# Kernel tuning notes

Measured on AMD Instinct MI355X. Metric: run time of the kernel, lower is better.

## Reference

```python
import jax, jax.numpy as jnp
import numpy as np

B, S, D, UNITS = 32, 2048, 1024, 1024


def setup_inputs() -> dict:
    key = jax.random.key(0)
    ks = jax.random.split(key, 8)
    scale_d = 1.0 / np.sqrt(D)
    scale_u = 1.0 / np.sqrt(UNITS)
    return {
        "query": jax.random.normal(ks[0], (B, D), jnp.float32),
        "values": jax.random.normal(ks[1], (B, S, D), jnp.float32),
        "W1": jax.random.normal(ks[2], (D, UNITS), jnp.float32) * scale_d,
        "b1": jnp.zeros((UNITS,), jnp.float32),
        "W2": jax.random.normal(ks[3], (D, UNITS), jnp.float32) * scale_d,
        "b2": jnp.zeros((UNITS,), jnp.float32),
        "V": jax.random.normal(ks[4], (UNITS, 1), jnp.float32) * scale_u,
        "bV": jnp.zeros((1,), jnp.float32),
    }


def reference(query, values, W1, b1, W2, b2, V, bV):
    # proj of encoder outputs: [B, S, UNITS]
    proj_v = jnp.einsum("bsd,du->bsu", values, W1) + b1
    # proj of query (hidden), broadcast over sequence: [B, 1, UNITS]
    proj_q = (query @ W2 + b2)[:, None, :]
    # scalar score per position: [B, S, 1]
    score = jnp.tanh(proj_v + proj_q) @ V + bV
    # softmax over the sequence axis (axis=1)
    attention_weights = jax.nn.softmax(score, axis=1)  # [B, S, 1]
    # weighted sum of values: [B, D]
    context_vector = jnp.sum(attention_weights * values, axis=1)
    return context_vector, attention_weights
```

## Files before the change

kernel.cpp:

```cpp
#include <hip/hip_runtime.h>
#include <stdint.h>

typedef float f32x4 __attribute__((ext_vector_type(4)));
typedef short bf16x8 __attribute__((ext_vector_type(8)));
typedef _Float16 f16x8 __attribute__((ext_vector_type(8)));

#define AS1 __attribute__((address_space(1)))
#define AS3 __attribute__((address_space(3)))

#define NB 32
#define NS 2048
#define ND 1024
#define NU 1024
#define NM (NB * NS)

__device__ __forceinline__ void glds16(const void* g, void* l) {
  __builtin_amdgcn_global_load_lds((const AS1 uint32_t*)g, (AS3 uint32_t*)l, 16, 0, 0);
}

__device__ __forceinline__ unsigned short bf16_rne(float f) {
  uint32_t u = __float_as_uint(f);
  u += 0x7fffu + ((u >> 16) & 1u);
  return (unsigned short)(u >> 16);
}

__device__ __forceinline__ uint32_t h2pack(float lo, float hi) {
  union { _Float16 h[2]; uint32_t u; } p;
  p.h[0] = (_Float16)lo;
  p.h[1] = (_Float16)hi;
  return p.u;
}

__device__ __forceinline__ uint32_t pack_bf16_trunc(float lo, float hi) {
  return __builtin_amdgcn_perm(__float_as_uint(hi), __float_as_uint(lo), 0x07060302u);
}

__device__ __forceinline__ float fast_tanh(float x) {
  float e = __expf(2.0f * x);
  return 1.0f - 2.0f / (e + 1.0f);
}

__global__ __launch_bounds__(256) void k_cvt(const float* __restrict__ values,
                                             _Float16* __restrict__ values_h) {
  const size_t gid = (size_t)blockIdx.x * 256 + threadIdx.x;
#pragma unroll 2
  for (int it = 0; it < 8; ++it) {
    const size_t e0 = gid * 8 + (size_t)it * 8388608;
    f32x4 v0 = *(const f32x4*)(values + e0);
    f32x4 v1 = *(const f32x4*)(values + e0 + 4);
    uint4 o;
    o.x = h2pack(v0.x, v0.y);
    o.y = h2pack(v0.z, v0.w);
    o.z = h2pack(v1.x, v1.y);
    o.w = h2pack(v1.z, v1.w);
    *(uint4*)(values_h + e0) = o;
  }
}

__global__ __launch_bounds__(256) void k_w1t_h(const float* __restrict__ W1,
                                               _Float16* __restrict__ W1T) {
  __shared__ float t[64][65];
  const int n0 = blockIdx.x * 64, k0 = blockIdx.y * 64;
  const int tid = threadIdx.x;
  {
    const int r = tid >> 4, c4 = (tid & 15) << 2;
#pragma unroll
    for (int i = 0; i < 4; ++i) {
      f32x4 v = *(const f32x4*)(W1 + (size_t)(k0 + r + i * 16) * NU + n0 + c4);
      t[r + i * 16][c4 + 0] = v.x;
      t[r + i * 16][c4 + 1] = v.y;
      t[r + i * 16][c4 + 2] = v.z;
      t[r + i * 16][c4 + 3] = v.w;
    }
  }
  __syncthreads();
  const int rr = tid >> 2, cc = tid & 3;
  uint32_t o[8];
#pragma unroll
  for (int p = 0; p < 8; ++p)
    o[p] = h2pack(t[cc * 16 + 2 * p + 0][rr], t[cc * 16 + 2 * p + 1][rr]);
  _Float16* dst = W1T + (size_t)(n0 + rr) * ND + k0 + cc * 16;
  *(uint4*)(dst + 0) = make_uint4(o[0], o[1], o[2], o[3]);
  *(uint4*)(dst + 8) = make_uint4(o[4], o[5], o[6], o[7]);
}

__global__ __launch_bounds__(256) void k_w1t(const float* __restrict__ W1,
                                             unsigned short* __restrict__ W1T) {
  __shared__ float t[64][65];
  const int n0 = blockIdx.x * 64, k0 = blockIdx.y * 64;
  const int tid = threadIdx.x;
  {
    const int r = tid >> 4, c4 = (tid & 15) << 2;
#pragma unroll
    for (int i = 0; i < 4; ++i) {
      f32x4 v = *(const f32x4*)(W1 + (size_t)(k0 + r + i * 16) * NU + n0 + c4);
      t[r + i * 16][c4 + 0] = v.x;
      t[r + i * 16][c4 + 1] = v.y;
      t[r + i * 16][c4 + 2] = v.z;
      t[r + i * 16][c4 + 3] = v.w;
    }
  }
  __syncthreads();
  const int rr = tid >> 2, cc = tid & 3;
  uint32_t o[8];
#pragma unroll
  for (int p = 0; p < 8; ++p) {
    float f0 = t[cc * 16 + 2 * p + 0][rr];
    float f1 = t[cc * 16 + 2 * p + 1][rr];
    o[p] = (uint32_t)bf16_rne(f0) | ((uint32_t)bf16_rne(f1) << 16);
  }
  unsigned short* dst = W1T + (size_t)(n0 + rr) * ND + k0 + cc * 16;
  *(uint4*)(dst + 0) = make_uint4(o[0], o[1], o[2], o[3]);
  *(uint4*)(dst + 8) = make_uint4(o[4], o[5], o[6], o[7]);
}

__global__ __launch_bounds__(256) void k_pq(const float* __restrict__ query,
                                            const float* __restrict__ W2,
                                            float* __restrict__ pq_part) {
  const int kc = blockIdx.x, b = blockIdx.y;
  const int u4 = threadIdx.x * 4;
  const float* q = query + b * ND + kc * 256;
  f32x4 a0 = (f32x4){0.f, 0.f, 0.f, 0.f}, a1 = a0;
  const float* w = W2 + (size_t)kc * 256 * NU + u4;
  for (int k = 0; k < 256; k += 8) {
#pragma unroll
    for (int j = 0; j < 8; j += 2) {
      a0 += q[k + j + 0] * *(const f32x4*)(w + (size_t)(k + j + 0) * NU);
      a1 += q[k + j + 1] * *(const f32x4*)(w + (size_t)(k + j + 1) * NU);
    }
  }
  *(f32x4*)(pq_part + (size_t)(kc * NB + b) * NU + u4) = a0 + a1;
}

__global__ __launch_bounds__(256) void k_pq_red(const float* __restrict__ pq_part,
                                                const float* __restrict__ b1,
                                                const float* __restrict__ b2,
                                                float* __restrict__ pq) {
  const int b = blockIdx.x, u4 = threadIdx.x * 4;
  f32x4 acc = *(const f32x4*)(b1 + u4) + *(const f32x4*)(b2 + u4);
#pragma unroll
  for (int kc = 0; kc < 4; ++kc)
    acc += *(const f32x4*)(pq_part + (size_t)(kc * NB + b) * NU + u4);
  *(f32x4*)(pq + (size_t)b * NU + u4) = acc;
}

__global__ __launch_bounds__(256) void k_score_h(const _Float16* __restrict__ valh,
                                                 const _Float16* __restrict__ W1T,
                                                 const float* __restrict__ pq,
                                                 const float* __restrict__ V,
                                                 float* __restrict__ score) {
  __shared__ f32x4 lds4[1024];
  char* lds = (char*)lds4;

  const int tid = threadIdx.x;
  const int lane = tid & 63;
  const int w = tid >> 6;
  const int wr = w >> 1, wc = w & 1;
  const int quad = lane >> 4, l15 = lane & 15;

  const int bid = blockIdx.x;
  const int xcd = bid & 7;
  const int local = bid >> 3;
  const int mt = xcd * 64 + (local >> 3);
  const int nc = local & 7;
  const int m0 = mt * 128, n0 = nc * 128;

  const char* aG[2];
  const char* bG[2];
  uint32_t aL[2], bL[2];
  {
    const int r = lane >> 2;
    const int ca = (lane & 3) ^ (r & 3);
#pragma unroll
    for (int i = 0; i < 2; ++i) {
      const int seg = w * 2 + i;
      const int rloc = seg * 16 + r;
      aG[i] = (const char*)valh + (size_t)(m0 + rloc) * (ND * 2) + ca * 16;
      aL[i] = seg * 1024;
      bG[i] = (const char*)W1T + (size_t)(n0 + rloc) * (ND * 2) + ca * 16;
      bL[i] = 8192 + seg * 1024;
    }
  }

  uint32_t aOff[4], bOff[4];
  {
    const int pp = (quad ^ (l15 & 3)) * 16;
#pragma unroll
    for (int ri = 0; ri < 4; ++ri) aOff[ri] = (wr * 64 + ri * 16 + l15) * 64 + pp;
#pragma unroll
    for (int ci = 0; ci < 4; ++ci) bOff[ci] = 8192 + (wc * 64 + ci * 16 + l15) * 64 + pp;
  }

  f32x4 acc[4][4];
#pragma unroll
  for (int i = 0; i < 4; ++i)
#pragma unroll
    for (int j = 0; j < 4; ++j) acc[i][j] = (f32x4){0.f, 0.f, 0.f, 0.f};

  for (int kt = 0; kt < 32; ++kt) {
    __syncthreads();
    const size_t col = (size_t)kt * 64;
#pragma unroll
    for (int i = 0; i < 2; ++i) glds16(aG[i] + col, lds + aL[i]);
#pragma unroll
    for (int i = 0; i < 2; ++i) glds16(bG[i] + col, lds + bL[i]);
    __syncthreads();

    f16x8 af[4], bf[4];
#pragma unroll
    for (int ri = 0; ri < 4; ++ri) {
      union { f32x4 f; f16x8 h; } u;
      u.f = *(const f32x4*)(lds + aOff[ri]);
      af[ri] = u.h;
    }
#pragma unroll
    for (int ci = 0; ci < 4; ++ci) {
      union { f32x4 f; f16x8 h; } u;
      u.f = *(const f32x4*)(lds + bOff[ci]);
      bf[ci] = u.h;
    }
#pragma unroll
    for (int ri = 0; ri < 4; ++ri)
#pragma unroll
      for (int ci = 0; ci < 4; ++ci)
        acc[ri][ci] =
            __builtin_amdgcn_mfma_f32_16x16x32_f16(af[ri], bf[ci], acc[ri][ci], 0, 0, 0);
  }

  const int b = m0 >> 11;
  float vv[4], qq[4];
#pragma unroll
  for (int ci = 0; ci < 4; ++ci) {
    const int col = n0 + wc * 64 + ci * 16 + l15;
    vv[ci] = V[col];
    qq[ci] = pq[b * NU + col];
  }
#pragma unroll
  for (int ri = 0; ri < 4; ++ri) {
    float p0 = 0.f, p1 = 0.f, p2 = 0.f, p3 = 0.f;
#pragma unroll
    for (int ci = 0; ci < 4; ++ci) {
      f32x4 a = acc[ri][ci];
      p0 += fast_tanh(a.x + qq[ci]) * vv[ci];
      p1 += fast_tanh(a.y + qq[ci]) * vv[ci];
      p2 += fast_tanh(a.z + qq[ci]) * vv[ci];
      p3 += fast_tanh(a.w + qq[ci]) * vv[ci];
    }
#pragma unroll
    for (int mask = 1; mask < 16; mask <<= 1) {
      p0 += __shfl_xor(p0, mask);
      p1 += __shfl_xor(p1, mask);
      p2 += __shfl_xor(p2, mask);
      p3 += __shfl_xor(p3, mask);
    }
    if (l15 == 0) {
      const int rbase = m0 + wr * 64 + ri * 16 + quad * 4;
      atomicAdd(&score[rbase + 0], p0);
      atomicAdd(&score[rbase + 1], p1);
      atomicAdd(&score[rbase + 2], p2);
      atomicAdd(&score[rbase + 3], p3);
    }
  }
}

__global__ __launch_bounds__(256) void k_score_f32(const float* __restrict__ values,
                                                   const unsigned short* __restrict__ W1T,
                                                   const float* __restrict__ pq,
                                                   const float* __restrict__ V,
                                                   float* __restrict__ score) {
  __shared__ f32x4 lds4[1536];
  char* lds = (char*)lds4;
  const int tid = threadIdx.x;
  const int lane = tid & 63;
  const int w = tid >> 6;
  const int wr = w >> 1, wc = w & 1;
  const int quad = lane >> 4, l15 = lane & 15;
  const int bid = blockIdx.x;
  const int xcd = bid & 7;
  const int local = bid >> 3;
  const int mt = xcd * 64 + (local >> 3);
  const int nc = local & 7;
  const int m0 = mt * 128, n0 = nc * 128;
  const char* aG[4];
  uint32_t aL[4];
  {
    const int p = lane & 7, r3 = lane >> 3;
    const int ca = p ^ r3;
#pragma unroll
    for (int i = 0; i < 4; ++i) {
      const int seg = w * 4 + i;
      const int mloc = seg * 8 + r3;
      aG[i] = (const char*)values + (size_t)(m0 + mloc) * (ND * 4) + ca * 16;
      aL[i] = seg * 1024;
    }
  }
  const char* bG[2];
  uint32_t bL[2];
  {
    const int cb = (lane & 3) ^ ((lane >> 3) & 3);
#pragma unroll
    for (int i = 0; i < 2; ++i) {
      const int seg = w * 2 + i;
      const int nloc = seg * 16 + (lane >> 2);
      bG[i] = (const char*)W1T + (size_t)(n0 + nloc) * (ND * 2) + cb * 16;
      bL[i] = 16384 + seg * 1024;
    }
  }
  uint32_t aOff[4][2], bOff[4];
  {
    const int p0 = (2 * quad) ^ (l15 & 7);
#pragma unroll
    for (int ri = 0; ri < 4; ++ri) {
      const int m = wr * 64 + ri * 16 + l15;
      aOff[ri][0] = m * 128 + p0 * 16;
      aOff[ri][1] = m * 128 + (p0 ^ 1) * 16;
    }
    const int pb = quad ^ ((l15 >> 1) & 3);
#pragma unroll
    for (int ci = 0; ci < 4; ++ci) {
      const int n = wc * 64 + ci * 16 + l15;
      bOff[ci] = 16384 + n * 64 + pb * 16;
    }
  }
  f32x4 acc[4][4];
#pragma unroll
  for (int i = 0; i < 4; ++i)
#pragma unroll
    for (int j = 0; j < 4; ++j) acc[i][j] = (f32x4){0.f, 0.f, 0.f, 0.f};
  for (int kt = 0; kt < 32; ++kt) {
    __syncthreads();
    const size_t aCol = (size_t)kt * 128;
    const size_t bCol = (size_t)kt * 64;
#pragma unroll
    for (int i = 0; i < 4; ++i) glds16(aG[i] + aCol, lds + aL[i]);
#pragma unroll
    for (int i = 0; i < 2; ++i) glds16(bG[i] + bCol, lds + bL[i]);
    __syncthreads();
    bf16x8 af[4];
#pragma unroll
    for (int ri = 0; ri < 4; ++ri) {
      f32x4 v0 = *(const f32x4*)(lds + aOff[ri][0]);
      f32x4 v1 = *(const f32x4*)(lds + aOff[ri][1]);
      union { uint32_t u[4]; bf16x8 v; } cvt;
      cvt.u[0] = pack_bf16_trunc(v0.x, v0.y);
      cvt.u[1] = pack_bf16_trunc(v0.z, v0.w);
      cvt.u[2] = pack_bf16_trunc(v1.x, v1.y);
      cvt.u[3] = pack_bf16_trunc(v1.z, v1.w);
      af[ri] = cvt.v;
    }
    bf16x8 bfg[4];
#pragma unroll
    for (int ci = 0; ci < 4; ++ci) {
      union { f32x4 f; bf16x8 v; } u;
      u.f = *(const f32x4*)(lds + bOff[ci]);
      bfg[ci] = u.v;
    }
#pragma unroll
    for (int ri = 0; ri < 4; ++ri)
#pragma unroll
      for (int ci = 0; ci < 4; ++ci)
        acc[ri][ci] =
            __builtin_amdgcn_mfma_f32_16x16x32_bf16(af[ri], bfg[ci], acc[ri][ci], 0, 0, 0);
  }
  const int b = m0 >> 11;
  float vv[4], qq[4];
#pragma unroll
  for (int ci = 0; ci < 4; ++ci) {
    const int col = n0 + wc * 64 + ci * 16 + l15;
    vv[ci] = V[col];
    qq[ci] = pq[b * NU + col];
  }
#pragma unroll
  for (int ri = 0; ri < 4; ++ri) {
    float p0 = 0.f, p1 = 0.f, p2 = 0.f, p3 = 0.f;
#pragma unroll
    for (int ci = 0; ci < 4; ++ci) {
      f32x4 a = acc[ri][ci];
      p0 += fast_tanh(a.x + qq[ci]) * vv[ci];
      p1 += fast_tanh(a.y + qq[ci]) * vv[ci];
      p2 += fast_tanh(a.z + qq[ci]) * vv[ci];
      p3 += fast_tanh(a.w + qq[ci]) * vv[ci];
    }
#pragma unroll
    for (int mask = 1; mask < 16; mask <<= 1) {
      p0 += __shfl_xor(p0, mask);
      p1 += __shfl_xor(p1, mask);
      p2 += __shfl_xor(p2, mask);
      p3 += __shfl_xor(p3, mask);
    }
    if (l15 == 0) {
      const int rbase = m0 + wr * 64 + ri * 16 + quad * 4;
      atomicAdd(&score[rbase + 0], p0);
      atomicAdd(&score[rbase + 1], p1);
      atomicAdd(&score[rbase + 2], p2);
      atomicAdd(&score[rbase + 3], p3);
    }
  }
}

__global__ __launch_bounds__(256) void k_softmax(const float* __restrict__ score,
                                                 float* __restrict__ attn) {
  __shared__ float red[8];
  const int b = blockIdx.x, tid = threadIdx.x;
  const int w = tid >> 6, lane = tid & 63;
  const float* s = score + b * NS;
  float v[8];
  float mx = -3.4e38f;
#pragma unroll
  for (int j = 0; j < 8; ++j) {
    v[j] = s[tid + j * 256];
    mx = fmaxf(mx, v[j]);
  }
#pragma unroll
  for (int mask = 1; mask < 64; mask <<= 1) mx = fmaxf(mx, __shfl_xor(mx, mask));
  if (lane == 0) red[w] = mx;
  __syncthreads();
  mx = fmaxf(fmaxf(red[0], red[1]), fmaxf(red[2], red[3]));
  float sum = 0.f;
#pragma unroll
  for (int j = 0; j < 8; ++j) {
    v[j] = __expf(v[j] - mx);
    sum += v[j];
  }
#pragma unroll
  for (int mask = 1; mask < 64; mask <<= 1) sum += __shfl_xor(sum, mask);
  if (lane == 0) red[4 + w] = sum;
  __syncthreads();
  const float inv = 1.0f / (red[4] + red[5] + red[6] + red[7]);
  float* o = attn + b * NS;
#pragma unroll
  for (int j = 0; j < 8; ++j) o[tid + j * 256] = v[j] * inv;
}

__global__ __launch_bounds__(128) void k_ctx_part_h(const _Float16* __restrict__ valh,
                                                    const float* __restrict__ attn,
                                                    float* __restrict__ part) {
  const int sc = blockIdx.x, b = blockIdx.y, t = threadIdx.x;
  const int row0 = b * NS + sc * 32;
  const int d8 = t * 8;
  const float* ab = attn + row0;
  float acc[8];
#pragma unroll
  for (int i = 0; i < 8; ++i) acc[i] = 0.f;
  for (int s0 = 0; s0 < 32; s0 += 8) {
    uint4 r[8];
#pragma unroll
    for (int j = 0; j < 8; ++j)
      r[j] = *(const uint4*)(valh + (size_t)(row0 + s0 + j) * ND + d8);
#pragma unroll
    for (int j = 0; j < 8; ++j) {
      union { uint4 u; _Float16 h[8]; } c;
      c.u = r[j];
      const float a = ab[s0 + j];
#pragma unroll
      for (int i = 0; i < 8; ++i) acc[i] = fmaf(a, (float)c.h[i], acc[i]);
    }
  }
  float* o = part + (size_t)(b * 64 + sc) * ND + d8;
#pragma unroll
  for (int i = 0; i < 8; ++i) o[i] = acc[i];
}

__global__ __launch_bounds__(256) void k_ctx_part_f32(const float* __restrict__ values,
                                                      const float* __restrict__ attn,
                                                      float* __restrict__ part) {
  const int sc = blockIdx.x, b = blockIdx.y, tid = threadIdx.x;
  const int s0 = sc * 64;
  const f32x4* vb = (const f32x4*)(values + (size_t)(b * NS + s0) * ND);
  const float* ab = attn + b * NS + s0;
  f32x4 acc0 = (f32x4){0.f, 0.f, 0.f, 0.f};
  f32x4 acc1 = acc0;
  for (int s = 0; s < 64; s += 8) {
    f32x4 v0 = vb[(size_t)(s + 0) * 256 + tid];
    f32x4 v1 = vb[(size_t)(s + 1) * 256 + tid];
    f32x4 v2 = vb[(size_t)(s + 2) * 256 + tid];
    f32x4 v3 = vb[(size_t)(s + 3) * 256 + tid];
    f32x4 v4 = vb[(size_t)(s + 4) * 256 + tid];
    f32x4 v5 = vb[(size_t)(s + 5) * 256 + tid];
    f32x4 v6 = vb[(size_t)(s + 6) * 256 + tid];
    f32x4 v7 = vb[(size_t)(s + 7) * 256 + tid];
    acc0 += ab[s + 0] * v0;
    acc1 += ab[s + 1] * v1;
    acc0 += ab[s + 2] * v2;
    acc1 += ab[s + 3] * v3;
    acc0 += ab[s + 4] * v4;
    acc1 += ab[s + 5] * v5;
    acc0 += ab[s + 6] * v6;
    acc1 += ab[s + 7] * v7;
  }
  *(f32x4*)(part + (size_t)(b * 32 + sc) * ND + tid * 4) = acc0 + acc1;
}

__global__ __launch_bounds__(256) void k_ctx_red(const float* __restrict__ part,
                                                 float* __restrict__ ctx, int count) {
  const int b = blockIdx.x, tid = threadIdx.x;
  f32x4 acc = (f32x4){0.f, 0.f, 0.f, 0.f};
  for (int sc = 0; sc < count; ++sc)
    acc += *(const f32x4*)(part + (size_t)(b * count + sc) * ND + tid * 4);
  *(f32x4*)(ctx + (size_t)b * ND + tid * 4) = acc;
}

extern "C" void kernel_launch(void* const* d_in, const int* in_sizes, int n_in,
                              void* d_out, int out_size, void* d_ws, size_t ws_size,
                              hipStream_t stream) {
  const float* query  = (const float*)d_in[0];
  const float* values = (const float*)d_in[1];
  const float* W1     = (const float*)d_in[2];
  const float* b1     = (const float*)d_in[3];
  const float* W2     = (const float*)d_in[4];
  const float* b2     = (const float*)d_in[5];
  const float* V      = (const float*)d_in[6];

  float* ctx  = (float*)d_out;
  float* attn = (float*)d_out + NB * ND;

  char* ws = (char*)d_ws;
  const size_t SZ_VALH = (size_t)NM * ND * 2;
  const size_t need_h = SZ_VALH + 2097152 + 524288 + 131072 + 262144 + 8388608;

  if (ws_size >= need_h) {
    _Float16* valh   = (_Float16*)ws;
    _Float16* W1Th   = (_Float16*)(ws + SZ_VALH);
    float* pq_part   = (float*)(ws + SZ_VALH + 2097152);
    float* pq        = (float*)(ws + SZ_VALH + 2621440);
    float* score     = (float*)(ws + SZ_VALH + 2752512);
    float* part      = (float*)(ws + SZ_VALH + 3014656);

    hipMemsetAsync(score, 0, NM * sizeof(float), stream);
    k_cvt<<<4096, 256, 0, stream>>>(values, valh);
    k_w1t_h<<<dim3(16, 16), 256, 0, stream>>>(W1, W1Th);
    k_pq<<<dim3(4, NB), 256, 0, stream>>>(query, W2, pq_part);
    k_pq_red<<<NB, 256, 0, stream>>>(pq_part, b1, b2, pq);
    k_score_h<<<4096, 256, 0, stream>>>(valh, W1Th, pq, V, score);
    k_softmax<<<NB, 256, 0, stream>>>(score, attn);
    k_ctx_part_h<<<dim3(64, NB), 128, 0, stream>>>(valh, attn, part);
    k_ctx_red<<<NB, 256, 0, stream>>>(part, ctx, 64);
  } else {
    unsigned short* W1T = (unsigned short*)ws;
    float* pq_part = (float*)(ws + 2097152);
    float* pq      = (float*)(ws + 2621440);
    float* score   = (float*)(ws + 2752512);
    float* part    = (float*)(ws + 3014656);

    hipMemsetAsync(score, 0, NM * sizeof(float), stream);
    k_w1t<<<dim3(16, 16), 256, 0, stream>>>(W1, W1T);
    k_pq<<<dim3(4, NB), 256, 0, stream>>>(query, W2, pq_part);
    k_pq_red<<<NB, 256, 0, stream>>>(pq_part, b1, b2, pq);
    k_score_f32<<<4096, 256, 0, stream>>>(values, W1T, pq, V, score);
    k_softmax<<<NB, 256, 0, stream>>>(score, attn);
    k_ctx_part_f32<<<dim3(32, NB), 256, 0, stream>>>(values, attn, part);
    k_ctx_red<<<NB, 256, 0, stream>>>(part, ctx, 32);
  }
}
```

Before: 662.2 us.

## Rewrite fp16 score GEMM as 256x256-tile, 8-wave, double-buffered pipelined kernel

New measurement: 655.9 us. About the same (-1.0%).

```diff
diff --git a/kernel.cpp b/kernel.cpp
--- a/kernel.cpp
+++ b/kernel.cpp
@@ -144,87 +144,173 @@
   *(f32x4*)(pq + (size_t)b * NU + u4) = acc;
 }
 
-__global__ __launch_bounds__(256) void k_score_h(const _Float16* __restrict__ valh,
+__global__ __launch_bounds__(512) void k_score_h(const _Float16* __restrict__ valh,
                                                  const _Float16* __restrict__ W1T,
                                                  const float* __restrict__ pq,
                                                  const float* __restrict__ V,
                                                  float* __restrict__ score) {
-  __shared__ f32x4 lds4[1024];
-  char* lds = (char*)lds4;
+  __shared__ f32x4 ldsv[8192];
+  char* lds = (char*)ldsv;
 
   const int tid = threadIdx.x;
   const int lane = tid & 63;
   const int w = tid >> 6;
-  const int wr = w >> 1, wc = w & 1;
+  const int wr = w >> 2;
+  const int wc = w & 3;
   const int quad = lane >> 4, l15 = lane & 15;
 
   const int bid = blockIdx.x;
-  const int xcd = bid & 7;
-  const int local = bid >> 3;
-  const int mt = xcd * 64 + (local >> 3);
-  const int nc = local & 7;
-  const int m0 = mt * 128, n0 = nc * 128;
-
-  const char* aG[2];
-  const char* bG[2];
-  uint32_t aL[2], bL[2];
-  {
-    const int r = lane >> 2;
-    const int ca = (lane & 3) ^ (r & 3);
-#pragma unroll
-    for (int i = 0; i < 2; ++i) {
-      const int seg = w * 2 + i;
-      const int rloc = seg * 16 + r;
-      aG[i] = (const char*)valh + (size_t)(m0 + rloc) * (ND * 2) + ca * 16;
-      aL[i] = seg * 1024;
-      bG[i] = (const char*)W1T + (size_t)(n0 + rloc) * (ND * 2) + ca * 16;
-      bL[i] = 8192 + seg * 1024;
-    }
-  }
-
-  uint32_t aOff[4], bOff[4];
-  {
-    const int pp = (quad ^ (l15 & 3)) * 16;
-#pragma unroll
-    for (int ri = 0; ri < 4; ++ri) aOff[ri] = (wr * 64 + ri * 16 + l15) * 64 + pp;
-#pragma unroll
-    for (int ci = 0; ci < 4; ++ci) bOff[ci] = 8192 + (wc * 64 + ci * 16 + l15) * 64 + pp;
-  }
-
-  f32x4 acc[4][4];
-#pragma unroll
-  for (int i = 0; i < 4; ++i)
+  const int sid = (bid & 7) * 128 + (bid >> 3);
+  const int mt = sid >> 2;
+  const int nc = sid & 3;
+  const int m0 = mt * 256, n0 = nc * 256;
+
+  const int r8 = lane >> 3, c8 = lane & 7;
+  const int colel = (c8 ^ r8) * 8;
+  const char* aS[2];
+  const char* bS[2];
+#pragma unroll
+  for (int i = 0; i < 2; ++i) {
+    const int seg = w * 2 + i;
+    aS[i] = (const char*)valh + ((size_t)(m0 + seg * 8 + r8) * ND + colel) * 2;
+    bS[i] = (const char*)W1T + ((size_t)(n0 + seg * 8 + r8) * ND + colel) * 2;
+  }
+  const int segL = w * 2048;
+
+#define STG_A(t, h, p)                                                                \
+  do {                                                                                \
+    glds16(aS[0] + (size_t)(h)*262144 + (size_t)(t)*128,                              \
+           lds + (p)*65536 + (h)*16384 + segL);                                       \
+    glds16(aS[1] + (size_t)(h)*262144 + (size_t)(t)*128,                              \
+           lds + (p)*65536 + (h)*16384 + segL + 1024);                                \
+  } while (0)
+#define STG_B(t, h, p)                                                                \
+  do {                                                                                \
+    glds16(bS[0] + (size_t)(h)*262144 + (size_t)(t)*128,                              \
+           lds + (p)*65536 + 32768 + (h)*16384 + segL);                               \
+    glds16(bS[1] + (size_t)(h)*262144 + (size_t)(t)*128,                              \
+           lds + (p)*65536 + 32768 + (h)*16384 + segL + 1024);                        \
+  } while (0)
+
+  const int xr0 = ((quad + 0) ^ (l15 & 7)) * 16;
+  const int xr1 = ((quad + 4) ^ (l15 & 7)) * 16;
+  const int aRow = (wr * 128 + l15) * 128;
+  const int bRow = 32768 + (wc * 64 + l15) * 128;
+
+  f16x8 af0[4][2], af1[4][2], bf[4][2];
+  f32x4 acc[8][4];
+#pragma unroll
+  for (int i = 0; i < 8; ++i)
 #pragma unroll
     for (int j = 0; j < 4; ++j) acc[i][j] = (f32x4){0.f, 0.f, 0.f, 0.f};
 
-  for (int kt = 0; kt < 32; ++kt) {
-    __syncthreads();
-    const size_t col = (size_t)kt * 64;
-#pragma unroll
-    for (int i = 0; i < 2; ++i) glds16(aG[i] + col, lds + aL[i]);
-#pragma unroll
-    for (int i = 0; i < 2; ++i) glds16(bG[i] + col, lds + bL[i]);
-    __syncthreads();
-
-    f16x8 af[4], bf[4];
-#pragma unroll
-    for (int ri = 0; ri < 4; ++ri) {
-      union { f32x4 f; f16x8 h; } u;
-      u.f = *(const f32x4*)(lds + aOff[ri]);
-      af[ri] = u.h;
-    }
-#pragma unroll
-    for (int ci = 0; ci < 4; ++ci) {
-      union { f32x4 f; f16x8 h; } u;
-      u.f = *(const f32x4*)(lds + bOff[ci]);
-      bf[ci] = u.h;
-    }
-#pragma unroll
-    for (int ri = 0; ri < 4; ++ri)
-#pragma unroll
-      for (int ci = 0; ci < 4; ++ci)
-        acc[ri][ci] =
-            __builtin_amdgcn_mfma_f32_16x16x32_f16(af[ri], bf[ci], acc[ri][ci], 0, 0, 0);
+#define LDA(dst, p, mq)                                                               \
+  do {                                                                                \
+    _Pragma("unroll") for (int fm = 0; fm < 4; ++fm) {                                \
+      const int rb = (p)*65536 + aRow + ((mq)*4 + fm) * 2048;                         \
+      dst[fm][0] = *(const f16x8*)(lds + rb + xr0);                                   \
+      dst[fm][1] = *(const f16x8*)(lds + rb + xr1);                                   \
+    }                                                                                 \
+  } while (0)
+#define LDB(p)                                                                        \
+  do {                                                                                \
+    _Pragma("unroll") for (int fn = 0; fn < 4; ++fn) {                                \
+      const int rb = (p)*65536 + bRow + fn * 2048;                                    \
+      bf[fn][0] = *(const f16x8*)(lds + rb + xr0);                                    \
+      bf[fn][1] = *(const f16x8*)(lds + rb + xr1);                                    \
+    }                                                                                 \
+  } while (0)
+#define MM(a, mq, nq)                                                                 \
+  do {                                                                                \
+    _Pragma("unroll") for (int fm = 0; fm < 4; ++fm) {                                \
+      _Pragma("unroll") for (int fn = 0; fn < 2; ++fn) {                              \
+        acc[(mq)*4 + fm][(nq)*2 + fn] = __builtin_amdgcn_mfma_f32_16x16x32_f16(       \
+            a[fm][0], bf[(nq)*2 + fn][0], acc[(mq)*4 + fm][(nq)*2 + fn], 0, 0, 0);    \
+        acc[(mq)*4 + fm][(nq)*2 + fn] = __builtin_amdgcn_mfma_f32_16x16x32_f16(       \
+            a[fm][1], bf[(nq)*2 + fn][1], acc[(mq)*4 + fm][(nq)*2 + fn], 0, 0, 0);    \
+      }                                                                               \
+    }                                                                                 \
+  } while (0)
+#define MIDBAR()                                                                      \
+  do {                                                                                \
+    __builtin_amdgcn_sched_barrier(0);                                                \
+    __builtin_amdgcn_s_barrier();                                                     \
+    asm volatile("s_waitcnt lgkmcnt(0)" ::: "memory");                                \
+    __builtin_amdgcn_sched_barrier(0);                                                \
+    __builtin_amdgcn_s_setprio(1);                                                    \
+  } while (0)
+#define ENDP()                                                                        \
+  do {                                                                                \
+    __builtin_amdgcn_s_setprio(0);                                                    \
+    __builtin_amdgcn_sched_barrier(0);                                                \
+    __builtin_amdgcn_s_barrier();                                                     \
+  } while (0)
+#define ENDPV()                                                                       \
+  do {                                                                                \
+    __builtin_amdgcn_s_setprio(0);                                                    \
+    __builtin_amdgcn_sched_barrier(0);                                                \
+    asm volatile("s_waitcnt vmcnt(4)" ::: "memory");                                  \
+    __builtin_amdgcn_s_barrier();                                                     \
+  } while (0)
+
+  STG_A(0, 0, 0);
+  STG_A(0, 1, 0);
+  STG_B(0, 0, 0);
+  STG_B(0, 1, 0);
+  STG_A(1, 0, 1);
+  STG_A(1, 1, 1);
+  asm volatile("s_waitcnt vmcnt(4)" ::: "memory");
+  __builtin_amdgcn_s_barrier();
+
+  for (int I = 0; I < 8; ++I) {
+    const int o = 2 * I + 1;
+    const int t2 = (2 * I + 2 < 16) ? 2 * I + 2 : 15;
+    const int t3 = (2 * I + 3 < 16) ? 2 * I + 3 : 15;
+    LDA(af0, 0, 0);
+    LDB(0);
+    STG_B(o, 0, 1);
+    MIDBAR();
+    MM(af0, 0, 0);
+    ENDP();
+
+    LDA(af1, 0, 1);
+    STG_B(o, 1, 1);
+    MIDBAR();
+    MM(af0, 0, 1);
+    ENDP();
+
+    STG_A(t2, 0, 0);
+    MIDBAR();
+    MM(af1, 1, 0);
+    ENDP();
+
+    STG_A(t2, 1, 0);
+    MIDBAR();
+    MM(af1, 1, 1);
+    ENDPV();
+
+    LDA(af0, 1, 0);
+    LDB(1);
+    STG_B(t2, 0, 0);
+    MIDBAR();
+    MM(af0, 0, 0);
+    ENDP();
+
+    LDA(af1, 1, 1);
+    STG_B(t2, 1, 0);
+    MIDBAR();
+    MM(af0, 0, 1);
+    ENDP();
+
+    STG_A(t3, 0, 1);
+    MIDBAR();
+    MM(af1, 1, 0);
+    ENDP();
+
+    STG_A(t3, 1, 1);
+    MIDBAR();
+    MM(af1, 1, 1);
+    ENDPV();
   }
 
   const int b = m0 >> 11;
@@ -236,7 +322,7 @@
     qq[ci] = pq[b * NU + col];
   }
 #pragma unroll
-  for (int ri = 0; ri < 4; ++ri) {
+  for (int ri = 0; ri < 8; ++ri) {
     float p0 = 0.f, p1 = 0.f, p2 = 0.f, p3 = 0.f;
 #pragma unroll
     for (int ci = 0; ci < 4; ++ci) {
@@ -254,13 +340,21 @@
       p3 += __shfl_xor(p3, mask);
     }
     if (l15 == 0) {
-      const int rbase = m0 + wr * 64 + ri * 16 + quad * 4;
+      const int rbase = m0 + wr * 128 + ri * 16 + quad * 4;
       atomicAdd(&score[rbase + 0], p0);
       atomicAdd(&score[rbase + 1], p1);
       atomicAdd(&score[rbase + 2], p2);
       atomicAdd(&score[rbase + 3], p3);
     }
   }
+#undef STG_A
+#undef STG_B
+#undef LDA
+#undef LDB
+#undef MM
+#undef MIDBAR
+#undef ENDP
+#undef ENDPV
 }
 
 __global__ __launch_bounds__(256) void k_score_f32(const float* __restrict__ values,
@@ -531,7 +625,7 @@
     k_w1t_h<<<dim3(16, 16), 256, 0, stream>>>(W1, W1Th);
     k_pq<<<dim3(4, NB), 256, 0, stream>>>(query, W2, pq_part);
     k_pq_red<<<NB, 256, 0, stream>>>(pq_part, b1, b2, pq);
-    k_score_h<<<4096, 256, 0, stream>>>(valh, W1Th, pq, V, score);
+    k_score_h<<<1024, 512, 0, stream>>>(valh, W1Th, pq, V, score);
     k_softmax<<<NB, 256, 0, stream>>>(score, attn);
     k_ctx_part_h<<<dim3(64, NB), 128, 0, stream>>>(valh, attn, part);
     k_ctx_red<<<NB, 256, 0, stream>>>(part, ctx, 64);
```
